# Performance work log

Measured on AMD Instinct MI355X. Metric: run time of the kernel, lower is better.

## Reference

```python
import jax, jax.numpy as jnp
import numpy as np

N = 100000      # nodes
E = 1600000     # directed edges (before self loops)
F_IN = 128      # n_features
H = 100         # hidden width of every GCNConv / fc1
N_HIDDEN = 8    # conv2..conv9


def setup_inputs() -> dict:
    key = jax.random.key(0)
    ks = jax.random.split(key, 12)
    s = 0.05
    x = jax.random.normal(ks[0], (N, F_IN), jnp.float32)
    edge_index = jax.random.randint(ks[1], (2, E), 0, N, dtype=jnp.int64)
    labels = (jax.random.uniform(ks[2], (N, 1)) < 0.1).astype(jnp.float32)
    W1 = jax.random.normal(ks[3], (F_IN, H), jnp.float32) * s
    b1 = jnp.zeros((H,), jnp.float32)
    Wh = jax.random.normal(ks[4], (N_HIDDEN, H, H), jnp.float32) * s
    bh = jnp.zeros((N_HIDDEN, H), jnp.float32)
    fc1_W = jax.random.normal(ks[5], (H, H), jnp.float32) * s
    fc1_b = jnp.zeros((H,), jnp.float32)
    fc2_W = jax.random.normal(ks[6], (H, 1), jnp.float32) * s
    fc2_b = jnp.zeros((1,), jnp.float32)
    return {"x": x, "edge_index": edge_index, "labels": labels,
            "W1": W1, "b1": b1, "Wh": Wh, "bh": bh,
            "fc1_W": fc1_W, "fc1_b": fc1_b, "fc2_W": fc2_W, "fc2_b": fc2_b}


def _gcn_conv(h, W, b, src, dst, norm):
    # linear transform, then degree-normalized scatter aggregation (PyG GCNConv)
    h = h @ W                                   # [N, H]
    msg = h[src] * norm[:, None]                # [E2, H] gather + scale
    agg = jax.ops.segment_sum(msg, dst, num_segments=N)  # scatter-add to [N, H]
    return agg + b


def reference(x, edge_index, labels, W1, b1, Wh, bh, fc1_W, fc1_b, fc2_W, fc2_b):
    # GCN normalization with self loops: norm_e = deg^-1/2[src] * deg^-1/2[dst]
    loops = jnp.arange(N, dtype=edge_index.dtype)
    src = jnp.concatenate([edge_index[0], loops])
    dst = jnp.concatenate([edge_index[1], loops])
    deg = jax.ops.segment_sum(jnp.ones_like(dst, jnp.float32), dst, num_segments=N)
    dinv = jax.lax.rsqrt(deg)                   # deg >= 1 due to self loops
    norm = dinv[src] * dinv[dst]

    # NOTE: source uses x.relu() (out-of-place, discarded) -> no nonlinearity;
    # dropout is identity in eval mode. Faithful reproduction below.
    h = _gcn_conv(x, W1, b1, src, dst, norm)
    for i in range(N_HIDDEN):
        h = _gcn_conv(h, Wh[i], bh[i], src, dst, norm)

    h = h @ fc1_W + fc1_b
    logits = h @ fc2_W + fc2_b
    p = jax.nn.sigmoid(logits)                  # [N, 1]

    # generate_weights: upweight positives by neg/pos ratio
    pos = labels.sum()
    w = ((jnp.float32(N) - pos) / pos) * labels + 1.0

    pc = jnp.clip(p, 1e-7, 1.0 - 1e-7)
    bce = -(labels * jnp.log(pc) + (1.0 - labels) * jnp.log(1.0 - pc))
    loss = jnp.mean(w * bce)
    return loss, p
```

## Files before the change

kernel.cpp:

```cpp
#include <hip/hip_runtime.h>
#include <hip/hip_fp16.h>
#include <math.h>

#define HW 100
#define FIN 128
#define NBLK 256
#define TPB 1024
#define CHUNK 392
#define PBLK 512
#define BCAP 64
#define ELDS 7424
#define M17 0x1FFFFu
#define NPADH 100352

typedef int iv4 __attribute__((ext_vector_type(4)));

__device__ __forceinline__ float ld_dev(const float* p) {
    return __hip_atomic_load(p, __ATOMIC_RELAXED, __HIP_MEMORY_SCOPE_AGENT);
}
__device__ __forceinline__ unsigned ld_devu(const unsigned* p) {
    return __hip_atomic_load(p, __ATOMIC_RELAXED, __HIP_MEMORY_SCOPE_AGENT);
}
__device__ __forceinline__ void st_devu(unsigned* p, unsigned v) {
    __hip_atomic_store(p, v, __ATOMIC_RELAXED, __HIP_MEMORY_SCOPE_AGENT);
}
__device__ __forceinline__ void st_devh(__half* p, __half v) {
    __hip_atomic_store(reinterpret_cast<unsigned short*>(p),
                       *reinterpret_cast<unsigned short*>(&v),
                       __ATOMIC_RELAXED, __HIP_MEMORY_SCOPE_AGENT);
}

__global__ void k_initchain(float* __restrict__ accums, unsigned* __restrict__ posDone,
                            unsigned* __restrict__ fin, unsigned* __restrict__ flags,
                            const float* __restrict__ W1, const float* __restrict__ b1,
                            const float* __restrict__ Wh, const float* __restrict__ bh,
                            const float* __restrict__ fc1W, const float* __restrict__ fc1b,
                            const float* __restrict__ fc2W, const float* __restrict__ fc2b,
                            float* __restrict__ wstar, float* __restrict__ gammas) {
    __shared__ float v[HW], vn[HW];
    int t = threadIdx.x;
    for (int i = t; i < NBLK * 16; i += 256) flags[i] = 0u;
    if (t < HW) v[t] = fc2W[t];
    __syncthreads();
    if (t < HW) { float a = 0.f; for (int c = 0; c < HW; ++c) a += fc1W[t * HW + c] * v[c]; vn[t] = a; }
    __syncthreads();
    if (t < HW) v[t] = vn[t];
    __syncthreads();
    if (t == 0) {
        float a = 0.f; for (int c = 0; c < HW; ++c) a += bh[7 * HW + c] * v[c];
        float b = 0.f; for (int c = 0; c < HW; ++c) b += fc1b[c] * fc2W[c];
        gammas[9] = a + b + fc2b[0];
    }
    __syncthreads();
    for (int i = 7; i >= 0; --i) {
        const float* M = Wh + (size_t)i * HW * HW;
        if (t < HW) { float a = 0.f; for (int c = 0; c < HW; ++c) a += M[t * HW + c] * v[c]; vn[t] = a; }
        __syncthreads();
        if (t < HW) v[t] = vn[t];
        __syncthreads();
        if (t == 0) {
            const float* bb = (i >= 1) ? (bh + (size_t)(i - 1) * HW) : b1;
            float a = 0.f; for (int c = 0; c < HW; ++c) a += bb[c] * v[c];
            gammas[i + 1] = a;
        }
        __syncthreads();
    }
    if (t < FIN) { float a = 0.f; for (int c = 0; c < HW; ++c) a += W1[t * HW + c] * v[c]; wstar[t] = a; }
    if (t == 0) { accums[0] = 0.f; accums[1] = 0.f; *posDone = 0u; *fin = 0u; }
}

__global__ __launch_bounds__(256) void k_part(const int* __restrict__ src,
                                              const int* __restrict__ dst, int E4,
                                              unsigned* __restrict__ buckets,
                                              int* __restrict__ cnt,
                                              const float* __restrict__ x,
                                              const float* __restrict__ wstar,
                                              float* __restrict__ y0raw, int N) {
    __shared__ int cur[NBLK];
    __shared__ float wsL[FIN];
    int tid = threadIdx.x;
    if (tid < NBLK) cur[tid] = 0;
    if (tid < FIN) wsL[tid] = wstar[tid];
    __syncthreads();
    const iv4* d4 = reinterpret_cast<const iv4*>(dst);
    const iv4* s4 = reinterpret_cast<const iv4*>(src);
    int i = blockIdx.x * 256 + tid;
    int stride = gridDim.x * 256;
    for (; i < E4; i += stride) {
        iv4 d = __builtin_nontemporal_load(d4 + i);
        iv4 s = __builtin_nontemporal_load(s4 + i);
        #pragma unroll
        for (int q = 0; q < 4; ++q) {
            unsigned dd = (unsigned)d[q];
            unsigned ss = (unsigned)s[q];
            unsigned c = (unsigned)(((unsigned long long)dd * 171634ull) >> 26);
            unsigned ldst = dd - c * 391u;
            int pos = atomicAdd(&cur[c], 1);
            if (pos < BCAP)
                buckets[((size_t)c * PBLK + blockIdx.x) * BCAP + pos] = ss | (ldst << 17);
        }
    }
    __syncthreads();
    if (tid < NBLK) cnt[(size_t)blockIdx.x * NBLK + tid] = cur[tid];

    int w = blockIdx.x * 4 + (tid >> 6);
    int lane = tid & 63;
    for (int r = w; r < N; r += PBLK * 4) {
        float2 xv = *reinterpret_cast<const float2*>(x + (size_t)r * FIN + lane * 2);
        float dsum = xv.x * wsL[lane * 2] + xv.y * wsL[lane * 2 + 1];
        #pragma unroll
        for (int off = 32; off; off >>= 1) dsum += __shfl_down(dsum, off);
        if (lane == 0) y0raw[r] = dsum;
    }
}

__global__ __launch_bounds__(TPB) void k_main(
        const float* __restrict__ labels,
        const float* __restrict__ y0raw, const float* __restrict__ gammas,
        const int* __restrict__ cntG, const unsigned* __restrict__ bucketsG,
        __half* __restrict__ ubase,
        float* __restrict__ accums, unsigned* __restrict__ flags,
        unsigned* __restrict__ posDone, unsigned* __restrict__ fin,
        float* __restrict__ outF, int N) {
    __shared__ float gam[16];
    __shared__ int   cntL[PBLK], incl[PBLK];
    __shared__ int   degLi[CHUNK];
    __shared__ float dinvL[CHUNK], uownL[CHUNK], yownL[CHUNK], accL[CHUNK];
    __shared__ float red[TPB];
    __shared__ alignas(16) unsigned myE[ELDS];

    int tid = threadIdx.x;
    int b = blockIdx.x;
    int chunk = (N + NBLK - 1) / NBLK;
    int nlo = b * chunk; if (nlo > N) nlo = N;
    int nhi = nlo + chunk; if (nhi > N) nhi = N;
    int nn = nhi - nlo;

    if (tid < 16) gam[tid] = gammas[tid];
    for (int r = tid; r < CHUNK; r += TPB) degLi[r] = 0;
    if (tid < PBLK) { int v = cntG[(size_t)tid * NBLK + b]; cntL[tid] = v; incl[tid] = v; }
    __syncthreads();
    for (int off = 1; off < PBLK; off <<= 1) {
        int v = (tid < PBLK && tid >= off) ? incl[tid - off] : 0;
        __syncthreads();
        if (tid < PBLK) incl[tid] += v;
        __syncthreads();
    }
    int ecnt = incl[PBLK - 1];
    if (ecnt > ELDS) ecnt = ELDS;

    const unsigned* col = bucketsG + (size_t)b * PBLK * BCAP;
    for (int idx = tid; idx < PBLK * BCAP; idx += TPB) {
        int p = idx >> 6, j = idx & (BCAP - 1);
        int c = cntL[p];
        if (j < c) {
            unsigned e = col[(size_t)p * BCAP + j];
            int o = incl[p] - c + j;
            if (o < ELDS) { myE[o] = e; atomicAdd(&degLi[e >> 17], 1); }
        }
    }
    __syncthreads();
    for (int r = tid; r < nn; r += TPB) dinvL[r] = rsqrtf((float)degLi[r] + 1.0f);
    __syncthreads();

    for (int ln = tid; ln < nn; ln += TPB) {
        float u0 = dinvL[ln] * y0raw[nlo + ln];
        uownL[ln] = u0;
        st_devh(&ubase[nlo + ln], __float2half(u0));
    }
    asm volatile("s_waitcnt vmcnt(0)" ::: "memory");
    {
        float s = 0.f;
        for (int ln = tid; ln < nn; ln += TPB) s += labels[nlo + ln];
        red[tid] = s; __syncthreads();
        for (int off = TPB / 2; off; off >>= 1) {
            if (tid < off) red[tid] += red[tid + off];
            __syncthreads();
        }
        if (tid == 0) {
            atomicAdd(&accums[0], red[0]);
            asm volatile("s_waitcnt vmcnt(0)" ::: "memory");
            __hip_atomic_fetch_add(posDone, 1u, __ATOMIC_RELAXED, __HIP_MEMORY_SCOPE_AGENT);
            st_devu(&flags[b * 16], 1u);
        }
    }

    for (int k = 1; k <= 9; ++k) {
        const __half* ubr = ubase + (size_t)(k - 1) * NPADH;
        __half* ubw = ubase + (size_t)k * NPADH;
        float gk = gam[k];
        for (int ln = tid; ln < nn; ln += TPB) accL[ln] = uownL[ln];
        if (tid < NBLK)
            while (ld_devu(&flags[tid * 16]) < (unsigned)k) __builtin_amdgcn_s_sleep(1);
        __syncthreads();
        int ecnt8 = ecnt & ~7;
        for (int e = tid * 8; e < ecnt8; e += TPB * 8) {
            uint4 pA = *reinterpret_cast<const uint4*>(&myE[e]);
            uint4 pB = *reinterpret_cast<const uint4*>(&myE[e + 4]);
            float f0 = __half2float(ubr[pA.x & M17]);
            float f1 = __half2float(ubr[pA.y & M17]);
            float f2 = __half2float(ubr[pA.z & M17]);
            float f3 = __half2float(ubr[pA.w & M17]);
            float f4 = __half2float(ubr[pB.x & M17]);
            float f5 = __half2float(ubr[pB.y & M17]);
            float f6 = __half2float(ubr[pB.z & M17]);
            float f7 = __half2float(ubr[pB.w & M17]);
            atomicAdd(&accL[pA.x >> 17], f0);
            atomicAdd(&accL[pA.y >> 17], f1);
            atomicAdd(&accL[pA.z >> 17], f2);
            atomicAdd(&accL[pA.w >> 17], f3);
            atomicAdd(&accL[pB.x >> 17], f4);
            atomicAdd(&accL[pB.y >> 17], f5);
            atomicAdd(&accL[pB.z >> 17], f6);
            atomicAdd(&accL[pB.w >> 17], f7);
        }
        for (int e = ecnt8 + tid; e < ecnt; e += TPB) {
            unsigned p = myE[e];
            atomicAdd(&accL[p >> 17], __half2float(ubr[p & M17]));
        }
        __syncthreads();
        for (int ln = tid; ln < nn; ln += TPB) {
            float di = dinvL[ln];
            float y = di * accL[ln] + gk;
            float nu = di * y;
            uownL[ln] = nu;
            if (k < 9) st_devh(&ubw[nlo + ln], __float2half(nu));
            else yownL[ln] = y;
        }
        if (k < 9) {
            asm volatile("s_waitcnt vmcnt(0)" ::: "memory");
            __syncthreads();
            if (tid == 0) st_devu(&flags[b * 16], (unsigned)(k + 1));
        }
    }
    __syncthreads();

    if (tid == 0)
        while (ld_devu(posDone) < NBLK) __builtin_amdgcn_s_sleep(2);
    __syncthreads();
    {
        float pos = ld_dev(&accums[0]);
        float wpos = ((float)N - pos) / pos;
        float acc = 0.f;
        for (int ln = tid; ln < nn; ln += TPB) {
            float y = yownL[ln];
            float pp = 1.f / (1.f + expf(-y));
            outF[1 + nlo + ln] = pp;
            float pc = fminf(fmaxf(pp, 1e-7f), 1.f - 1e-7f);
            float l = labels[nlo + ln];
            float w = wpos * l + 1.f;
            acc += w * (-(l * logf(pc) + (1.f - l) * logf(1.f - pc)));
        }
        red[tid] = acc; __syncthreads();
        for (int off = TPB / 2; off; off >>= 1) {
            if (tid < off) red[tid] += red[tid + off];
            __syncthreads();
        }
        if (tid == 0) {
            atomicAdd(&accums[1], red[0]);
            asm volatile("s_waitcnt vmcnt(0)" ::: "memory");
            unsigned old = __hip_atomic_fetch_add(fin, 1u, __ATOMIC_RELAXED, __HIP_MEMORY_SCOPE_AGENT);
            if (old == NBLK - 1u)
                outF[0] = ld_dev(&accums[1]) / (float)N;
        }
    }
}

extern "C" void kernel_launch(void* const* d_in, const int* in_sizes, int n_in,
                              void* d_out, int out_size, void* d_ws, size_t ws_size,
                              hipStream_t stream) {
    const float* x      = (const float*)d_in[0];
    const int*   edge   = (const int*)d_in[1];
    const float* labels = (const float*)d_in[2];
    const float* W1     = (const float*)d_in[3];
    const float* b1     = (const float*)d_in[4];
    const float* Wh     = (const float*)d_in[5];
    const float* bh     = (const float*)d_in[6];
    const float* fc1W   = (const float*)d_in[7];
    const float* fc1b   = (const float*)d_in[8];
    const float* fc2W   = (const float*)d_in[9];
    const float* fc2b   = (const float*)d_in[10];

    const int N = in_sizes[0] / FIN;
    const int E = in_sizes[1] / 2;
    const int* srcIdx = edge;
    const int* dstIdx = edge + E;

    size_t o = 0;
    auto carve = [&](size_t bytes) {
        void* p = (char*)d_ws + o;
        o += (bytes + 511) & ~(size_t)511;
        return p;
    };
    float*    accums  = (float*)   carve(4 * 4);
    unsigned* posDone = (unsigned*)carve(4);
    unsigned* fin     = (unsigned*)carve(4);
    unsigned* flags   = (unsigned*)carve((size_t)NBLK * 16 * 4);
    float*    wstar   = (float*)   carve(FIN * 4);
    float*    gammas  = (float*)   carve(16 * 4);
    float*    y0raw   = (float*)   carve((size_t)N * 4);
    __half*   ubase   = (__half*)  carve((size_t)NPADH * 10 * 2);
    int*      cnt     = (int*)     carve((size_t)PBLK * NBLK * 4);
    unsigned* buckets = (unsigned*)carve((size_t)NBLK * PBLK * BCAP * 4);
    (void)ws_size; (void)n_in; (void)out_size;

    k_initchain<<<1, 256, 0, stream>>>(accums, posDone, fin, flags,
                                       W1, b1, Wh, bh, fc1W, fc1b, fc2W, fc2b,
                                       wstar, gammas);
    k_part<<<PBLK, 256, 0, stream>>>(srcIdx, dstIdx, E / 4, buckets, cnt,
                                     x, wstar, y0raw, N);

    float* outF = (float*)d_out;
    int Nv = N;
    void* args[] = {(void*)&labels, (void*)&y0raw, (void*)&gammas,
                    (void*)&cnt, (void*)&buckets, (void*)&ubase,
                    (void*)&accums, (void*)&flags, (void*)&posDone, (void*)&fin,
                    (void*)&outF, (void*)&Nv};
    hipError_t err = hipLaunchCooperativeKernel((const void*)k_main, dim3(NBLK), dim3(TPB),
                                                args, 0, stream);
    (void)err;
}
```

Measured before the change: 222.0 us.

## Merge weight-chain into partition kernel and fuse x·w* projection into main

The single-block weight-chain kernel becomes block 0 of the edge partition kernel, so it runs alongside the bucketing instead of serialising before it. The projection of x onto the collapsed weight vector moves out of the partition kernel into the cooperative main kernel, where each block computes its own nodes directly. This drops a kernel launch and the y0raw round trip through global memory. In exchange, the main kernel now streams the 51 MB x matrix inside its prologue, which could lengthen the cooperative kernel.

```diff
diff --git a/kernel.cpp b/kernel.cpp
--- a/kernel.cpp
+++ b/kernel.cpp
@@ -30,62 +30,60 @@
                        __ATOMIC_RELAXED, __HIP_MEMORY_SCOPE_AGENT);
 }
 
-__global__ void k_initchain(float* __restrict__ accums, unsigned* __restrict__ posDone,
-                            unsigned* __restrict__ fin, unsigned* __restrict__ flags,
-                            const float* __restrict__ W1, const float* __restrict__ b1,
-                            const float* __restrict__ Wh, const float* __restrict__ bh,
-                            const float* __restrict__ fc1W, const float* __restrict__ fc1b,
-                            const float* __restrict__ fc2W, const float* __restrict__ fc2b,
-                            float* __restrict__ wstar, float* __restrict__ gammas) {
-    __shared__ float v[HW], vn[HW];
-    int t = threadIdx.x;
-    for (int i = t; i < NBLK * 16; i += 256) flags[i] = 0u;
-    if (t < HW) v[t] = fc2W[t];
-    __syncthreads();
-    if (t < HW) { float a = 0.f; for (int c = 0; c < HW; ++c) a += fc1W[t * HW + c] * v[c]; vn[t] = a; }
-    __syncthreads();
-    if (t < HW) v[t] = vn[t];
-    __syncthreads();
-    if (t == 0) {
-        float a = 0.f; for (int c = 0; c < HW; ++c) a += bh[7 * HW + c] * v[c];
-        float b = 0.f; for (int c = 0; c < HW; ++c) b += fc1b[c] * fc2W[c];
-        gammas[9] = a + b + fc2b[0];
-    }
-    __syncthreads();
-    for (int i = 7; i >= 0; --i) {
-        const float* M = Wh + (size_t)i * HW * HW;
-        if (t < HW) { float a = 0.f; for (int c = 0; c < HW; ++c) a += M[t * HW + c] * v[c]; vn[t] = a; }
-        __syncthreads();
-        if (t < HW) v[t] = vn[t];
-        __syncthreads();
-        if (t == 0) {
-            const float* bb = (i >= 1) ? (bh + (size_t)(i - 1) * HW) : b1;
-            float a = 0.f; for (int c = 0; c < HW; ++c) a += bb[c] * v[c];
-            gammas[i + 1] = a;
-        }
-        __syncthreads();
-    }
-    if (t < FIN) { float a = 0.f; for (int c = 0; c < HW; ++c) a += W1[t * HW + c] * v[c]; wstar[t] = a; }
-    if (t == 0) { accums[0] = 0.f; accums[1] = 0.f; *posDone = 0u; *fin = 0u; }
-}
-
-__global__ __launch_bounds__(256) void k_part(const int* __restrict__ src,
+__global__ __launch_bounds__(256) void k_prep(const int* __restrict__ src,
                                               const int* __restrict__ dst, int E4,
                                               unsigned* __restrict__ buckets,
                                               int* __restrict__ cnt,
-                                              const float* __restrict__ x,
-                                              const float* __restrict__ wstar,
-                                              float* __restrict__ y0raw, int N) {
+                                              float* __restrict__ accums,
+                                              unsigned* __restrict__ posDone,
+                                              unsigned* __restrict__ fin,
+                                              unsigned* __restrict__ flags,
+                                              const float* __restrict__ W1, const float* __restrict__ b1,
+                                              const float* __restrict__ Wh, const float* __restrict__ bh,
+                                              const float* __restrict__ fc1W, const float* __restrict__ fc1b,
+                                              const float* __restrict__ fc2W, const float* __restrict__ fc2b,
+                                              float* __restrict__ wstar, float* __restrict__ gammas) {
+    int tid = threadIdx.x;
+    if (blockIdx.x == 0) {
+        __shared__ float v[HW], vn[HW];
+        for (int i = tid; i < NBLK * 16; i += 256) flags[i] = 0u;
+        if (tid < HW) v[tid] = fc2W[tid];
+        __syncthreads();
+        if (tid < HW) { float a = 0.f; for (int c = 0; c < HW; ++c) a += fc1W[tid * HW + c] * v[c]; vn[tid] = a; }
+        __syncthreads();
+        if (tid < HW) v[tid] = vn[tid];
+        __syncthreads();
+        if (tid == 0) {
+            float a = 0.f; for (int c = 0; c < HW; ++c) a += bh[7 * HW + c] * v[c];
+            float b = 0.f; for (int c = 0; c < HW; ++c) b += fc1b[c] * fc2W[c];
+            gammas[9] = a + b + fc2b[0];
+        }
+        __syncthreads();
+        for (int i = 7; i >= 0; --i) {
+            const float* M = Wh + (size_t)i * HW * HW;
+            if (tid < HW) { float a = 0.f; for (int c = 0; c < HW; ++c) a += M[tid * HW + c] * v[c]; vn[tid] = a; }
+            __syncthreads();
+            if (tid < HW) v[tid] = vn[tid];
+            __syncthreads();
+            if (tid == 0) {
+                const float* bb = (i >= 1) ? (bh + (size_t)(i - 1) * HW) : b1;
+                float a = 0.f; for (int c = 0; c < HW; ++c) a += bb[c] * v[c];
+                gammas[i + 1] = a;
+            }
+            __syncthreads();
+        }
+        if (tid < FIN) { float a = 0.f; for (int c = 0; c < HW; ++c) a += W1[tid * HW + c] * v[c]; wstar[tid] = a; }
+        if (tid == 0) { accums[0] = 0.f; accums[1] = 0.f; *posDone = 0u; *fin = 0u; }
+        return;
+    }
     __shared__ int cur[NBLK];
-    __shared__ float wsL[FIN];
-    int tid = threadIdx.x;
+    int pb = blockIdx.x - 1;
     if (tid < NBLK) cur[tid] = 0;
-    if (tid < FIN) wsL[tid] = wstar[tid];
     __syncthreads();
     const iv4* d4 = reinterpret_cast<const iv4*>(dst);
     const iv4* s4 = reinterpret_cast<const iv4*>(src);
-    int i = blockIdx.x * 256 + tid;
-    int stride = gridDim.x * 256;
+    int i = pb * 256 + tid;
+    int stride = PBLK * 256;
     for (; i < E4; i += stride) {
         iv4 d = __builtin_nontemporal_load(d4 + i);
         iv4 s = __builtin_nontemporal_load(s4 + i);
@@ -97,31 +95,22 @@
             unsigned ldst = dd - c * 391u;
             int pos = atomicAdd(&cur[c], 1);
             if (pos < BCAP)
-                buckets[((size_t)c * PBLK + blockIdx.x) * BCAP + pos] = ss | (ldst << 17);
-        }
-    }
-    __syncthreads();
-    if (tid < NBLK) cnt[(size_t)blockIdx.x * NBLK + tid] = cur[tid];
-
-    int w = blockIdx.x * 4 + (tid >> 6);
-    int lane = tid & 63;
-    for (int r = w; r < N; r += PBLK * 4) {
-        float2 xv = *reinterpret_cast<const float2*>(x + (size_t)r * FIN + lane * 2);
-        float dsum = xv.x * wsL[lane * 2] + xv.y * wsL[lane * 2 + 1];
-        #pragma unroll
-        for (int off = 32; off; off >>= 1) dsum += __shfl_down(dsum, off);
-        if (lane == 0) y0raw[r] = dsum;
-    }
-}
-
-__global__ __launch_bounds__(TPB) void k_main(
+                buckets[((size_t)c * PBLK + pb) * BCAP + pos] = ss | (ldst << 17);
+        }
+    }
+    __syncthreads();
+    if (tid < NBLK) cnt[(size_t)pb * NBLK + tid] = cur[tid];
+}
+
+__global__ __launch_bounds__(TPB) void k_main(const float* __restrict__ x,
         const float* __restrict__ labels,
-        const float* __restrict__ y0raw, const float* __restrict__ gammas,
+        const float* __restrict__ wstar, const float* __restrict__ gammas,
         const int* __restrict__ cntG, const unsigned* __restrict__ bucketsG,
         __half* __restrict__ ubase,
         float* __restrict__ accums, unsigned* __restrict__ flags,
         unsigned* __restrict__ posDone, unsigned* __restrict__ fin,
         float* __restrict__ outF, int N) {
+    __shared__ alignas(16) float ws[FIN];
     __shared__ float gam[16];
     __shared__ int   cntL[PBLK], incl[PBLK];
     __shared__ int   degLi[CHUNK];
@@ -136,6 +125,7 @@
     int nhi = nlo + chunk; if (nhi > N) nhi = N;
     int nn = nhi - nlo;
 
+    if (tid < FIN) ws[tid] = wstar[tid];
     if (tid < 16) gam[tid] = gammas[tid];
     for (int r = tid; r < CHUNK; r += TPB) degLi[r] = 0;
     if (tid < PBLK) { int v = cntG[(size_t)tid * NBLK + b]; cntL[tid] = v; incl[tid] = v; }
@@ -163,10 +153,26 @@
     for (int r = tid; r < nn; r += TPB) dinvL[r] = rsqrtf((float)degLi[r] + 1.0f);
     __syncthreads();
 
-    for (int ln = tid; ln < nn; ln += TPB) {
-        float u0 = dinvL[ln] * y0raw[nlo + ln];
-        uownL[ln] = u0;
-        st_devh(&ubase[nlo + ln], __float2half(u0));
+    {
+        int wid = tid >> 6, half = (tid >> 5) & 1, l32 = tid & 31;
+        int pcnt = (nn + 1) >> 1;
+        const float4* x4 = reinterpret_cast<const float4*>(x);
+        for (int pb = wid; pb < pcnt; pb += 16) {
+            int ln = pb * 2 + half;
+            float dsum = 0.f;
+            if (ln < nn) {
+                float4 xv = x4[(size_t)(nlo + ln) * (FIN / 4) + l32];
+                float4 wv = *reinterpret_cast<const float4*>(&ws[l32 * 4]);
+                dsum = xv.x * wv.x + xv.y * wv.y + xv.z * wv.z + xv.w * wv.w;
+            }
+            #pragma unroll
+            for (int off = 16; off; off >>= 1) dsum += __shfl_down(dsum, off, 32);
+            if (l32 == 0 && ln < nn) {
+                float u0 = dsum * dinvL[ln];
+                uownL[ln] = u0;
+                st_devh(&ubase[nlo + ln], __float2half(u0));
+            }
+        }
     }
     asm volatile("s_waitcnt vmcnt(0)" ::: "memory");
     {
@@ -298,21 +304,19 @@
     unsigned* flags   = (unsigned*)carve((size_t)NBLK * 16 * 4);
     float*    wstar   = (float*)   carve(FIN * 4);
     float*    gammas  = (float*)   carve(16 * 4);
-    float*    y0raw   = (float*)   carve((size_t)N * 4);
     __half*   ubase   = (__half*)  carve((size_t)NPADH * 10 * 2);
     int*      cnt     = (int*)     carve((size_t)PBLK * NBLK * 4);
     unsigned* buckets = (unsigned*)carve((size_t)NBLK * PBLK * BCAP * 4);
     (void)ws_size; (void)n_in; (void)out_size;
 
-    k_initchain<<<1, 256, 0, stream>>>(accums, posDone, fin, flags,
-                                       W1, b1, Wh, bh, fc1W, fc1b, fc2W, fc2b,
-                                       wstar, gammas);
-    k_part<<<PBLK, 256, 0, stream>>>(srcIdx, dstIdx, E / 4, buckets, cnt,
-                                     x, wstar, y0raw, N);
+    k_prep<<<PBLK + 1, 256, 0, stream>>>(srcIdx, dstIdx, E / 4, buckets, cnt,
+                                         accums, posDone, fin, flags,
+                                         W1, b1, Wh, bh, fc1W, fc1b, fc2W, fc2b,
+                                         wstar, gammas);
 
     float* outF = (float*)d_out;
     int Nv = N;
-    void* args[] = {(void*)&labels, (void*)&y0raw, (void*)&gammas,
+    void* args[] = {(void*)&x, (void*)&labels, (void*)&wstar, (void*)&gammas,
                     (void*)&cnt, (void*)&buckets, (void*)&ubase,
                     (void*)&accums, (void*)&flags, (void*)&posDone, (void*)&fin,
                     (void*)&outF, (void*)&Nv};
```

Result: faster. 197.4 us (-11.1%).
